# Kernel optimization log

Measured on AMD Instinct MI355X. Metric: run time of the kernel, lower is better.

The kernel has to match this reference:

```python
import jax, jax.numpy as jnp
import numpy as np

B, D, M, K = 4096, 768, 100000, 10


def setup_inputs() -> dict:
    key = jax.random.key(0)
    k1, k2 = jax.random.split(key)
    x = jax.random.normal(k1, (B, D), dtype=jnp.float32)
    evidence_embeddings = jax.random.normal(k2, (M, D), dtype=jnp.float32)
    return {"x": x, "evidence_embeddings": evidence_embeddings, "k": K}


def reference(x, evidence_embeddings, k):
    # cos_sim = x @ E^T  -> [B, M]
    cos_sim = jnp.einsum("bd,md->bm", x, evidence_embeddings)
    # top-k along evidence dim (dim=1)
    scores, indices = jax.lax.top_k(cos_sim, k)
    return scores, indices
```

## Files before the change

### kernel.cpp

```cpp
#include <hip/hip_runtime.h>
#include <math.h>
#include <stdint.h>

#define B_ROWS 4096
#define D_DIM  768
#define M_ROWS 100000
#define K_TOP  10

#define KSTEPS 48
#define E32N   3125
#define B32N   128
#define NGRP   16
#define NBB    16
#define NITER_TOT 391
#define CAND   12
#define KCN    12
#define LTK    6

typedef _Float16 f16;
typedef _Float16 f16x8 __attribute__((ext_vector_type(8)));
typedef float   f32x16 __attribute__((ext_vector_type(16)));

#define XF_BYTES (128ull * 48 * 1024)
#define EF_OFF   XF_BYTES
#define EF_BYTES (3125ull * 48 * 1024)
#define CS_OFF   (EF_OFF + EF_BYTES)
#define CS_BYTES (4096ull * NGRP * CAND * 4)
#define CI_OFF   (CS_OFF + CS_BYTES)
#define CI_BYTES (4096ull * NGRP * CAND * 4)
#define WS_NEED  (CI_OFF + CI_BYTES)

__global__ __launch_bounds__(256) void convert_frag(
    const float* __restrict__ src, f16* __restrict__ dst, int nband)
{
  int tid  = blockIdx.x * 256 + threadIdx.x;
  int l    = tid & 63;
  int rest = tid >> 6;
  int ks   = rest % KSTEPS;
  int band = rest / KSTEPS;
  if (band >= nband) return;
  int row = band * 32 + (l & 31);
  int k0  = ks * 16 + 8 * (l >> 5);
  const float* s = src + (size_t)row * D_DIM + k0;
  float4 v0 = *(const float4*)s;
  float4 v1 = *(const float4*)(s + 4);
  f16x8 o;
  o[0] = (f16)v0.x; o[1] = (f16)v0.y; o[2] = (f16)v0.z; o[3] = (f16)v0.w;
  o[4] = (f16)v1.x; o[5] = (f16)v1.y; o[6] = (f16)v1.z; o[7] = (f16)v1.w;
  *(f16x8*)(dst + (((size_t)band * KSTEPS + ks) << 9) + l * 8) = o;
}

__device__ __forceinline__ void ins6(float (&ts)[LTK], int (&ti)[LTK],
                                     float s, int idx)
{
  ts[LTK - 1] = s; ti[LTK - 1] = idx;
#pragma unroll
  for (int q = LTK - 1; q > 0; --q) {
    if (ts[q] > ts[q - 1]) {
      float a = ts[q]; ts[q] = ts[q - 1]; ts[q - 1] = a;
      int   b = ti[q]; ti[q] = ti[q - 1]; ti[q - 1] = b;
    }
  }
}

__device__ __forceinline__ float max16(const f32x16& v)
{
  float a = fmaxf(fmaxf(v[0], v[1]), fmaxf(v[2], v[3]));
  float b = fmaxf(fmaxf(v[4], v[5]), fmaxf(v[6], v[7]));
  float c = fmaxf(fmaxf(v[8], v[9]), fmaxf(v[10], v[11]));
  float d = fmaxf(fmaxf(v[12], v[13]), fmaxf(v[14], v[15]));
  return fmaxf(fmaxf(a, b), fmaxf(c, d));
}

__global__ __launch_bounds__(512, 2) void gemm_topk(
    const f16* __restrict__ Ef, const f16* __restrict__ Xf,
    float* __restrict__ cs, int* __restrict__ ci)
{
  __shared__ f16 lds[2][32768];

  const int t    = threadIdx.x;
  const int lane = t & 63;
  const int w    = t >> 6;
  const int ew   = w >> 2;
  const int bw   = w & 3;

  const int id = blockIdx.x;
  const int g  = (id & 7) + 8 * (id >> 7);
  const int bb = (id >> 3) & 15;
  const int niter = 24 + (g < (NITER_TOT - 16 * 24) ? 1 : 0);

  const bool isE = (w < 4);
  const f16* xsrc0 = Xf + (((size_t)(bb * 8 + 2 * (w - 4)) * KSTEPS) << 9);
  const f16* xsrc1 = Xf + (((size_t)(bb * 8 + 2 * (w - 4) + 1) * KSTEPS) << 9);
  const uint32_t dstE0 = (isE ? (2 * w) * 2048 : 16384 + 2 * (w - 4) * 2048);
  const uint32_t dstE1 = dstE0 + 2048;

  float ts0[LTK], ts1[LTK]; int ti0[LTK], ti1[LTK];
#pragma unroll
  for (int q = 0; q < LTK; ++q) {
    ts0[q] = -INFINITY; ts1[q] = -INFINITY;
    ti0[q] = 0x7fffffff; ti1[q] = 0x7fffffff;
  }

  for (int j = 0; j < niter; ++j) {
    const int it = g + NGRP * j;
    const int e32base = it * 8;

    const f16 *s0, *s1;
    if (isE) {
      int ea = e32base + 2 * w;     if (ea > E32N - 1) ea = E32N - 1;
      int eb = e32base + 2 * w + 1; if (eb > E32N - 1) eb = E32N - 1;
      s0 = Ef + (((size_t)ea * KSTEPS) << 9);
      s1 = Ef + (((size_t)eb * KSTEPS) << 9);
    } else { s0 = xsrc0; s1 = xsrc1; }

    f32x16 acc0[4], acc1[4];
#pragma unroll
    for (int e = 0; e < 4; ++e) {
#pragma unroll
      for (int q = 0; q < 16; ++q) { acc0[e][q] = 0.f; acc1[e][q] = 0.f; }
    }

    auto STAGE = [&](int kc, int bufi) {
      const f16* a0 = s0 + ((size_t)kc << 11) + lane * 8;
      const f16* a1 = s1 + ((size_t)kc << 11) + lane * 8;
      f16* d0 = &lds[bufi][0] + dstE0 + lane * 8;
      f16* d1 = &lds[bufi][0] + dstE1 + lane * 8;
#pragma unroll
      for (int ff = 0; ff < 4; ++ff) {
        __builtin_amdgcn_global_load_lds(
            (const __attribute__((address_space(1))) void*)(uintptr_t)(a0 + ff * 512),
            (__attribute__((address_space(3))) void*)(uint32_t)(uintptr_t)(d0 + ff * 512),
            16, 0, 0);
      }
#pragma unroll
      for (int ff = 0; ff < 4; ++ff) {
        __builtin_amdgcn_global_load_lds(
            (const __attribute__((address_space(1))) void*)(uintptr_t)(a1 + ff * 512),
            (__attribute__((address_space(3))) void*)(uint32_t)(uintptr_t)(d1 + ff * 512),
            16, 0, 0);
      }
    };

    STAGE(0, 0);
    for (int kc = 0; kc < KCN; ++kc) {
      asm volatile("s_waitcnt vmcnt(0)" ::: "memory");
      __builtin_amdgcn_s_barrier();
      if (kc < KCN - 1) STAGE(kc + 1, (kc + 1) & 1);
      const f16* Lb = &lds[kc & 1][0];
#pragma unroll
      for (int kk = 0; kk < 4; ++kk) {
        f16x8 a[4], b[2];
#pragma unroll
        for (int e = 0; e < 4; ++e)
          a[e] = *(const f16x8*)(Lb + ((((ew * 4 + e) * 4 + kk)) << 9) + lane * 8);
#pragma unroll
        for (int x2 = 0; x2 < 2; ++x2)
          b[x2] = *(const f16x8*)(Lb + ((32 + (bw * 2 + x2) * 4 + kk) << 9) + lane * 8);
#pragma unroll
        for (int e = 0; e < 4; ++e) {
          acc0[e] = __builtin_amdgcn_mfma_f32_32x32x16_f16(a[e], b[0], acc0[e], 0, 0, 0);
          acc1[e] = __builtin_amdgcn_mfma_f32_32x32x16_f16(a[e], b[1], acc1[e], 0, 0, 0);
        }
      }
    }

#pragma unroll
    for (int e = 0; e < 4; ++e) {
      const int ebase = e32base * 32 + (ew * 4 + e) * 32 + 4 * (lane >> 5);
      if (max16(acc0[e]) > ts0[LTK - 1]) {
#pragma unroll
        for (int q = 0; q < 16; ++q) {
          int eidx = ebase + (q & 3) + 8 * (q >> 2);
          float s = acc0[e][q];
          if (eidx < M_ROWS && s > ts0[LTK - 1]) ins6(ts0, ti0, s, eidx);
        }
      }
      if (max16(acc1[e]) > ts1[LTK - 1]) {
#pragma unroll
        for (int q = 0; q < 16; ++q) {
          int eidx = ebase + (q & 3) + 8 * (q >> 2);
          float s = acc1[e][q];
          if (eidx < M_ROWS && s > ts1[LTK - 1]) ins6(ts1, ti1, s, eidx);
        }
      }
    }
  }

  __syncthreads();
  float* ds = (float*)&lds[0][0];
  int*   di = (int*)((char*)&lds[0][0] + 32 * 1024);
  {
    int half = lane >> 5, cl = lane & 31;
    int base0 = ((((ew * 2 + half) * 4 + bw) * 2 + 0) * 32 + cl) * LTK;
    int base1 = ((((ew * 2 + half) * 4 + bw) * 2 + 1) * 32 + cl) * LTK;
#pragma unroll
    for (int q = 0; q < LTK; ++q) {
      ds[base0 + q] = ts0[q]; di[base0 + q] = ti0[q];
      ds[base1 + q] = ts1[q]; di[base1 + q] = ti1[q];
    }
  }
  __syncthreads();
  if (t < 256) {
    int c = t; int bw2 = c >> 6, bt2 = (c >> 5) & 1, cl2 = c & 31;
    int hb[4];
#pragma unroll
    for (int u = 0; u < 4; ++u) {
      int ew2 = u >> 1, h2 = u & 1;
      hb[u] = ((((ew2 * 2 + h2) * 4 + bw2) * 2 + bt2) * 32 + cl2) * LTK;
    }
    const int row = bb * 256 + c;
    float* ocs = cs + ((size_t)row * NGRP + g) * CAND;
    int*   oci = ci + ((size_t)row * NGRP + g) * CAND;
    for (int o = 0; o < CAND; ++o) {
      float best = -INFINITY; int bidx = 0x7fffffff; int bu = 0, bq = 0;
#pragma unroll
      for (int u = 0; u < 4; ++u) {
        for (int q = 0; q < LTK; ++q) {
          float s = ds[hb[u] + q]; int id2 = di[hb[u] + q];
          if (s > best || (s == best && id2 < bidx)) { best = s; bidx = id2; bu = u; bq = q; }
        }
      }
      ds[hb[bu] + bq] = -INFINITY;
      ocs[o] = best; oci[o] = bidx;
    }
  }
}

__global__ __launch_bounds__(64) void final_merge(
    const float* __restrict__ x, const float* __restrict__ E,
    const float* __restrict__ cs, const int* __restrict__ ci,
    float* __restrict__ out)
{
  __shared__ float ls[192]; __shared__ int li[192];
  __shared__ int c16[16]; __shared__ double rs[16];
  const int row = blockIdx.x;
  const int lane = threadIdx.x;
  for (int q = lane; q < 192; q += 64) {
    ls[q] = cs[(size_t)row * 192 + q];
    li[q] = ci[(size_t)row * 192 + q];
  }
  __syncthreads();

  for (int o = 0; o < 16; ++o) {
    float bs = -INFINITY; int bi = 0x7fffffff; int bp = 0;
    for (int q = lane; q < 192; q += 64) {
      float s = ls[q];
      if (s > bs || (s == bs && li[q] < bi)) { bs = s; bi = li[q]; bp = q; }
    }
#pragma unroll
    for (int mk = 1; mk <= 32; mk <<= 1) {
      float qs = __shfl_xor(bs, mk, 64);
      int   qi = __shfl_xor(bi, mk, 64);
      int   qp = __shfl_xor(bp, mk, 64);
      if (qs > bs || (qs == bs && qi < bi)) { bs = qs; bi = qi; bp = qp; }
    }
    if (lane == 0) { c16[o] = bi; ls[bp] = -INFINITY; }
    __syncthreads();
  }

  {
    int cd = lane >> 2, p = lane & 3;
    int cid = c16[cd];
    const float* Er = E + (size_t)cid * D_DIM + p * 192;
    const float* Xr = x + (size_t)row * D_DIM + p * 192;
    double s = 0.0;
#pragma unroll 8
    for (int d = 0; d < 192; ++d) s += (double)Xr[d] * (double)Er[d];
    s += __shfl_xor(s, 1, 64);
    s += __shfl_xor(s, 2, 64);
    if (p == 0) rs[cd] = s;
  }
  __syncthreads();

  if (lane == 0) {
    for (int o = 0; o < K_TOP; ++o) {
      double bs = rs[0]; int bc = c16[0]; int b = 0;
      for (int q = 1; q < 16; ++q) {
        double v = rs[q]; int cq = c16[q];
        if (v > bs || (v == bs && cq < bc)) { bs = v; bc = cq; b = q; }
      }
      out[(size_t)row * K_TOP + o] = (float)bs;
      out[(size_t)B_ROWS * K_TOP + (size_t)row * K_TOP + o] = (float)bc;
      rs[b] = -1.0e300;
    }
  }
}

#define RB   16
#define GQ   64
#define MMF  4
#define NJ   391
#define NTF  1024
#define XPAD 772
#define DQ4  192

__global__ __launch_bounds__(NTF, 4) void retr_fused(
    const float* __restrict__ x, const float* __restrict__ E,
    float* __restrict__ out)
{
  __shared__ float smem[21248];
  const int t = threadIdx.x;
  const int r = t & 15;
  const int g = t >> 4;
  const int rb0 = blockIdx.x * RB;
  {
    const float4* xg = (const float4*)(x + (size_t)rb0 * D_DIM);
    for (int q = t; q < RB * DQ4; q += NTF) {
      int row = q / DQ4, c4 = q % DQ4;
      float4 v = xg[q];
      *(float4*)(smem + row * XPAD + c4 * 4) = v;
    }
  }
  __syncthreads();
  float ts[K_TOP]; int ti[K_TOP];
#pragma unroll
  for (int q = 0; q < K_TOP; ++q) { ts[q] = -INFINITY; ti[q] = 0x7fffffff; }
  const float4* xr4 = (const float4*)(smem + r * XPAD);
  for (int j = 0; j < NJ; ++j) {
    const int m0 = (g + (j << 6)) * MMF;
    const float4* ep[MMF];
#pragma unroll
    for (int mm = 0; mm < MMF; ++mm) {
      int ml = m0 + mm;
      int mc = (ml < M_ROWS) ? ml : (M_ROWS - 1);
      ep[mm] = (const float4*)(E + (size_t)mc * D_DIM);
    }
    float4 acc[MMF];
#pragma unroll
    for (int mm = 0; mm < MMF; ++mm) acc[mm] = make_float4(0.f, 0.f, 0.f, 0.f);
#pragma unroll 4
    for (int dq = 0; dq < DQ4; ++dq) {
      float4 xv = xr4[dq];
#pragma unroll
      for (int mm = 0; mm < MMF; ++mm) {
        float4 e = ep[mm][dq];
        acc[mm].x += e.x * xv.x; acc[mm].y += e.y * xv.y;
        acc[mm].z += e.z * xv.z; acc[mm].w += e.w * xv.w;
      }
    }
#pragma unroll
    for (int mm = 0; mm < MMF; ++mm) {
      int ml = m0 + mm;
      float s = (acc[mm].x + acc[mm].y) + (acc[mm].z + acc[mm].w);
      if (ml < M_ROWS && s > ts[K_TOP - 1]) {
        ts[K_TOP - 1] = s; ti[K_TOP - 1] = ml;
#pragma unroll
        for (int q = K_TOP - 1; q > 0; --q) {
          if (ts[q] > ts[q - 1]) {
            float tf = ts[q]; ts[q] = ts[q - 1]; ts[q - 1] = tf;
            int   tq = ti[q]; ti[q] = ti[q - 1]; ti[q - 1] = tq;
          }
        }
      }
    }
  }
  __syncthreads();
  float*  cs  = smem;
  int*    ci  = (int*)(smem + 10240);
  int*    cnd = (int*)(smem + 20480);
  double* rsd = (double*)(smem + 20736);
#pragma unroll
  for (int q = 0; q < K_TOP; ++q) {
    cs[(r * GQ + g) * K_TOP + q] = ts[q];
    ci[(r * GQ + g) * K_TOP + q] = ti[q];
  }
  __syncthreads();
  const int w = t >> 6;
  const int lane = t & 63;
  {
    float ms[K_TOP]; int mi[K_TOP];
#pragma unroll
    for (int q = 0; q < K_TOP; ++q) {
      ms[q] = cs[(w * GQ + lane) * K_TOP + q];
      mi[q] = ci[(w * GQ + lane) * K_TOP + q];
    }
    for (int o = 0; o < 16; ++o) {
      float hs = ms[0]; int hi = mi[0];
      float bs = hs;    int bi = hi;
#pragma unroll
      for (int mk = 1; mk <= 32; mk <<= 1) {
        float qs = __shfl_xor(bs, mk, 64);
        int   qi = __shfl_xor(bi, mk, 64);
        if (qs > bs || (qs == bs && qi < bi)) { bs = qs; bi = qi; }
      }
      bool win = (hs == bs) && (hi == bi);
      if (win) {
#pragma unroll
        for (int q = 0; q < K_TOP - 1; ++q) { ms[q] = ms[q + 1]; mi[q] = mi[q + 1]; }
        ms[K_TOP - 1] = -INFINITY; mi[K_TOP - 1] = 0x7fffffff;
      }
      if (lane == 0) cnd[w * 16 + o] = bi;
    }
  }
  __syncthreads();
  {
    int cand = lane >> 2, p = lane & 3;
    int cid = cnd[w * 16 + cand];
    const float* Er = E + (size_t)cid * D_DIM + p * 192;
    const float* Xr = x + (size_t)(rb0 + w) * D_DIM + p * 192;
    double s = 0.0;
#pragma unroll 8
    for (int d = 0; d < 192; ++d) s += (double)Xr[d] * (double)Er[d];
    s += __shfl_xor(s, 1, 64);
    s += __shfl_xor(s, 2, 64);
    if (p == 0) rsd[w * 16 + cand] = s;
  }
  __syncthreads();
  if (lane == 0) {
    const int row = rb0 + w;
    for (int o = 0; o < K_TOP; ++o) {
      double bsv = rsd[w * 16 + 0]; int bci = cnd[w * 16 + 0]; int b = 0;
      for (int q = 1; q < 16; ++q) {
        double v = rsd[w * 16 + q]; int c = cnd[w * 16 + q];
        if (v > bsv || (v == bsv && c < bci)) { bsv = v; bci = c; b = q; }
      }
      out[(size_t)row * K_TOP + o] = (float)bsv;
      out[(size_t)B_ROWS * K_TOP + (size_t)row * K_TOP + o] = (float)bci;
      rsd[w * 16 + b] = -1.0e300;
    }
  }
}

extern "C" void kernel_launch(void* const* d_in, const int* in_sizes, int n_in,
                              void* d_out, int out_size, void* d_ws, size_t ws_size,
                              hipStream_t stream) {
  const float* x = (const float*)d_in[0];
  const float* E = (const float*)d_in[1];
  float* out = (float*)d_out;

  if (ws_size < WS_NEED) {
    retr_fused<<<dim3(B_ROWS / RB), NTF, 0, stream>>>(x, E, out);
    return;
  }

  f16*   Xfp = (f16*)d_ws;
  f16*   Efp = (f16*)((char*)d_ws + EF_OFF);
  float* csp = (float*)((char*)d_ws + CS_OFF);
  int*   cip = (int*)((char*)d_ws + CI_OFF);

  convert_frag<<<dim3((B32N * KSTEPS * 64) / 256), 256, 0, stream>>>(x, Xfp, B32N);
  convert_frag<<<dim3((E32N * KSTEPS * 64) / 256), 256, 0, stream>>>(E, Efp, E32N);
  gemm_topk<<<dim3(NBB * NGRP), 512, 0, stream>>>(Efp, Xfp, csp, cip);
  final_merge<<<dim3(B_ROWS), 64, 0, stream>>>(x, E, csp, cip, out);
}
```

Baseline: 941.5 us.

## Deepen LDS pipeline to four stages and prefetch across tile iterations

Splits the K loop into 24 smaller chunks held in a 4-buffer LDS ring. Loads are issued three stages ahead, including the first chunks of the next E tile, so they overlap the current tile's top-k epilogue. Partial vmcnt waits replace the full drain on each step. It also raises wave priority around the MFMA bursts. The cost is twice as many barriers per tile and more complex waitcnt bookkeeping at the loop tail.

```diff
diff --git a/kernel.cpp b/kernel.cpp
--- a/kernel.cpp
+++ b/kernel.cpp
@@ -14,7 +14,7 @@
 #define NBB    16
 #define NITER_TOT 391
 #define CAND   12
-#define KCN    12
+#define KCN    24
 #define LTK    6
 
 typedef _Float16 f16;
@@ -72,11 +72,19 @@
   return fmaxf(fmaxf(a, b), fmaxf(c, d));
 }
 
+__device__ __forceinline__ void gll16(const f16* src, f16* dst)
+{
+  __builtin_amdgcn_global_load_lds(
+      (const __attribute__((address_space(1))) void*)(uintptr_t)src,
+      (__attribute__((address_space(3))) void*)(uint32_t)(uintptr_t)dst,
+      16, 0, 0);
+}
+
 __global__ __launch_bounds__(512, 2) void gemm_topk(
     const f16* __restrict__ Ef, const f16* __restrict__ Xf,
     float* __restrict__ cs, int* __restrict__ ci)
 {
-  __shared__ f16 lds[2][32768];
+  __shared__ f16 lds[4][16384];
 
   const int t    = threadIdx.x;
   const int lane = t & 63;
@@ -90,10 +98,27 @@
   const int niter = 24 + (g < (NITER_TOT - 16 * 24) ? 1 : 0);
 
   const bool isE = (w < 4);
-  const f16* xsrc0 = Xf + (((size_t)(bb * 8 + 2 * (w - 4)) * KSTEPS) << 9);
-  const f16* xsrc1 = Xf + (((size_t)(bb * 8 + 2 * (w - 4) + 1) * KSTEPS) << 9);
-  const uint32_t dstE0 = (isE ? (2 * w) * 2048 : 16384 + 2 * (w - 4) * 2048);
-  const uint32_t dstE1 = dstE0 + 2048;
+  const f16* xs0 = Xf + ((size_t)(bb * 8 + 2 * (w - 4)) * KSTEPS) * 512;
+  const f16* xs1 = Xf + ((size_t)(bb * 8 + 2 * (w - 4) + 1) * KSTEPS) * 512;
+  const uint32_t dbase = (isE ? (4 * w) * 512 : (16 + 4 * (w - 4)) * 512);
+
+  auto STAGE = [&](int e32b, int kc, int bufi) {
+    const f16 *s0, *s1;
+    if (isE) {
+      int ea = e32b + 2 * w;     if (ea > E32N - 1) ea = E32N - 1;
+      int eb = e32b + 2 * w + 1; if (eb > E32N - 1) eb = E32N - 1;
+      s0 = Ef + ((size_t)ea * KSTEPS + 2 * kc) * 512;
+      s1 = Ef + ((size_t)eb * KSTEPS + 2 * kc) * 512;
+    } else {
+      s0 = xs0 + (size_t)(2 * kc) * 512;
+      s1 = xs1 + (size_t)(2 * kc) * 512;
+    }
+    f16* dp = &lds[bufi][0] + dbase + lane * 8;
+    gll16(s0 + lane * 8,       dp);
+    gll16(s0 + lane * 8 + 512, dp + 512);
+    gll16(s1 + lane * 8,       dp + 1024);
+    gll16(s1 + lane * 8 + 512, dp + 1536);
+  };
 
   float ts0[LTK], ts1[LTK]; int ti0[LTK], ti1[LTK];
 #pragma unroll
@@ -102,17 +127,13 @@
     ti0[q] = 0x7fffffff; ti1[q] = 0x7fffffff;
   }
 
+  STAGE(g * 8, 0, 0);
+  STAGE(g * 8, 1, 1);
+  STAGE(g * 8, 2, 2);
+
   for (int j = 0; j < niter; ++j) {
-    const int it = g + NGRP * j;
-    const int e32base = it * 8;
-
-    const f16 *s0, *s1;
-    if (isE) {
-      int ea = e32base + 2 * w;     if (ea > E32N - 1) ea = E32N - 1;
-      int eb = e32base + 2 * w + 1; if (eb > E32N - 1) eb = E32N - 1;
-      s0 = Ef + (((size_t)ea * KSTEPS) << 9);
-      s1 = Ef + (((size_t)eb * KSTEPS) << 9);
-    } else { s0 = xsrc0; s1 = xsrc1; }
+    const int e32base = (g + NGRP * j) * 8;
+    const bool lastj = (j == niter - 1);
 
     f32x16 acc0[4], acc1[4];
 #pragma unroll
@@ -121,47 +142,37 @@
       for (int q = 0; q < 16; ++q) { acc0[e][q] = 0.f; acc1[e][q] = 0.f; }
     }
 
-    auto STAGE = [&](int kc, int bufi) {
-      const f16* a0 = s0 + ((size_t)kc << 11) + lane * 8;
-      const f16* a1 = s1 + ((size_t)kc << 11) + lane * 8;
-      f16* d0 = &lds[bufi][0] + dstE0 + lane * 8;
-      f16* d1 = &lds[bufi][0] + dstE1 + lane * 8;
-#pragma unroll
-      for (int ff = 0; ff < 4; ++ff) {
-        __builtin_amdgcn_global_load_lds(
-            (const __attribute__((address_space(1))) void*)(uintptr_t)(a0 + ff * 512),
-            (__attribute__((address_space(3))) void*)(uint32_t)(uintptr_t)(d0 + ff * 512),
-            16, 0, 0);
-      }
-#pragma unroll
-      for (int ff = 0; ff < 4; ++ff) {
-        __builtin_amdgcn_global_load_lds(
-            (const __attribute__((address_space(1))) void*)(uintptr_t)(a1 + ff * 512),
-            (__attribute__((address_space(3))) void*)(uint32_t)(uintptr_t)(d1 + ff * 512),
-            16, 0, 0);
-      }
-    };
-
-    STAGE(0, 0);
+#pragma unroll 1
     for (int kc = 0; kc < KCN; ++kc) {
-      asm volatile("s_waitcnt vmcnt(0)" ::: "memory");
+      if (!lastj || kc < KCN - 2) {
+        asm volatile("s_waitcnt vmcnt(8)" ::: "memory");
+      } else if (kc == KCN - 2) {
+        asm volatile("s_waitcnt vmcnt(4)" ::: "memory");
+      } else {
+        asm volatile("s_waitcnt vmcnt(0)" ::: "memory");
+      }
       __builtin_amdgcn_s_barrier();
-      if (kc < KCN - 1) STAGE(kc + 1, (kc + 1) & 1);
-      const f16* Lb = &lds[kc & 1][0];
-#pragma unroll
-      for (int kk = 0; kk < 4; ++kk) {
+
+      if (kc < KCN - 3)      STAGE(e32base, kc + 3, (kc + 3) & 3);
+      else if (!lastj)       STAGE(e32base + NGRP * 8, kc + 3 - KCN, (kc + 3) & 3);
+
+      const f16* Lb = &lds[kc & 3][0];
+#pragma unroll
+      for (int u = 0; u < 2; ++u) {
         f16x8 a[4], b[2];
 #pragma unroll
         for (int e = 0; e < 4; ++e)
-          a[e] = *(const f16x8*)(Lb + ((((ew * 4 + e) * 4 + kk)) << 9) + lane * 8);
+          a[e] = *(const f16x8*)(Lb + (((ew * 4 + e) * 2 + u) << 9) + lane * 8);
 #pragma unroll
         for (int x2 = 0; x2 < 2; ++x2)
-          b[x2] = *(const f16x8*)(Lb + ((32 + (bw * 2 + x2) * 4 + kk) << 9) + lane * 8);
+          b[x2] = *(const f16x8*)(Lb + ((16 + (bw * 2 + x2) * 2 + u) << 9) + lane * 8);
+        __builtin_amdgcn_s_setprio(1);
 #pragma unroll
         for (int e = 0; e < 4; ++e) {
           acc0[e] = __builtin_amdgcn_mfma_f32_32x32x16_f16(a[e], b[0], acc0[e], 0, 0, 0);
           acc1[e] = __builtin_amdgcn_mfma_f32_32x32x16_f16(a[e], b[1], acc1[e], 0, 0, 0);
         }
+        __builtin_amdgcn_s_setprio(0);
       }
     }
 
```

Measured after the change: 1.184 ms. +25.7%, slower.

## Load X fragments directly to registers, stage only E via LDS, remap blocks to XCDs

Applied to the files above, without the earlier changes.

X operand fragments are now read straight from global memory into registers each k-chunk instead of being staged through LDS. Only E tiles go through LDS, so the LDS buffer is halved and all 8 waves share E staging with 4 loads each. The block-to-(bb,g) mapping is reorganised so each XCD covers a subset of X row blocks and E groups, aiming for better L2 locality. A bounds clamp on candidate indices in the refinement kernel is added for safety.

```diff
diff --git a/kernel.cpp b/kernel.cpp
--- a/kernel.cpp
+++ b/kernel.cpp
@@ -72,11 +72,19 @@
   return fmaxf(fmaxf(a, b), fmaxf(c, d));
 }
 
+__device__ __forceinline__ void gll16(const f16* src, f16* dst)
+{
+  __builtin_amdgcn_global_load_lds(
+      (const __attribute__((address_space(1))) void*)(uintptr_t)src,
+      (__attribute__((address_space(3))) void*)(uint32_t)(uintptr_t)dst,
+      16, 0, 0);
+}
+
 __global__ __launch_bounds__(512, 2) void gemm_topk(
     const f16* __restrict__ Ef, const f16* __restrict__ Xf,
     float* __restrict__ cs, int* __restrict__ ci)
 {
-  __shared__ f16 lds[2][32768];
+  __shared__ f16 lds[2][16384];
 
   const int t    = threadIdx.x;
   const int lane = t & 63;
@@ -84,16 +92,17 @@
   const int ew   = w >> 2;
   const int bw   = w & 3;
 
-  const int id = blockIdx.x;
-  const int g  = (id & 7) + 8 * (id >> 7);
-  const int bb = (id >> 3) & 15;
+  const int id  = blockIdx.x;
+  const int xcd = id & 7;
+  const int q8  = id >> 3;
+  const int bb  = 8 * (xcd >> 2) + (q8 & 7);
+  const int g   = 4 * (xcd & 3) + (q8 >> 3);
   const int niter = 24 + (g < (NITER_TOT - 16 * 24) ? 1 : 0);
 
-  const bool isE = (w < 4);
-  const f16* xsrc0 = Xf + (((size_t)(bb * 8 + 2 * (w - 4)) * KSTEPS) << 9);
-  const f16* xsrc1 = Xf + (((size_t)(bb * 8 + 2 * (w - 4) + 1) * KSTEPS) << 9);
-  const uint32_t dstE0 = (isE ? (2 * w) * 2048 : 16384 + 2 * (w - 4) * 2048);
-  const uint32_t dstE1 = dstE0 + 2048;
+  const uint32_t dbase = (uint32_t)(w * 4) * 512;
+
+  const f16* xb0 = Xf + ((size_t)(bb * 8 + bw * 2 + 0) * KSTEPS) * 512 + lane * 8;
+  const f16* xb1 = Xf + ((size_t)(bb * 8 + bw * 2 + 1) * KSTEPS) * 512 + lane * 8;
 
   float ts0[LTK], ts1[LTK]; int ti0[LTK], ti1[LTK];
 #pragma unroll
@@ -103,16 +112,16 @@
   }
 
   for (int j = 0; j < niter; ++j) {
-    const int it = g + NGRP * j;
-    const int e32base = it * 8;
-
-    const f16 *s0, *s1;
-    if (isE) {
-      int ea = e32base + 2 * w;     if (ea > E32N - 1) ea = E32N - 1;
-      int eb = e32base + 2 * w + 1; if (eb > E32N - 1) eb = E32N - 1;
-      s0 = Ef + (((size_t)ea * KSTEPS) << 9);
-      s1 = Ef + (((size_t)eb * KSTEPS) << 9);
-    } else { s0 = xsrc0; s1 = xsrc1; }
+    const int e32base = (g + NGRP * j) * 8;
+
+    auto STAGE = [&](int kc, int bufi) {
+      int et = e32base + w; if (et > E32N - 1) et = E32N - 1;
+      const f16* s0 = Ef + ((size_t)et * KSTEPS + kc * 4) * 512 + lane * 8;
+      f16* d0 = &lds[bufi][0] + dbase + lane * 8;
+#pragma unroll
+      for (int ff = 0; ff < 4; ++ff)
+        gll16(s0 + ff * 512, d0 + ff * 512);
+    };
 
     f32x16 acc0[4], acc1[4];
 #pragma unroll
@@ -120,47 +129,33 @@
 #pragma unroll
       for (int q = 0; q < 16; ++q) { acc0[e][q] = 0.f; acc1[e][q] = 0.f; }
     }
-
-    auto STAGE = [&](int kc, int bufi) {
-      const f16* a0 = s0 + ((size_t)kc << 11) + lane * 8;
-      const f16* a1 = s1 + ((size_t)kc << 11) + lane * 8;
-      f16* d0 = &lds[bufi][0] + dstE0 + lane * 8;
-      f16* d1 = &lds[bufi][0] + dstE1 + lane * 8;
-#pragma unroll
-      for (int ff = 0; ff < 4; ++ff) {
-        __builtin_amdgcn_global_load_lds(
-            (const __attribute__((address_space(1))) void*)(uintptr_t)(a0 + ff * 512),
-            (__attribute__((address_space(3))) void*)(uint32_t)(uintptr_t)(d0 + ff * 512),
-            16, 0, 0);
-      }
-#pragma unroll
-      for (int ff = 0; ff < 4; ++ff) {
-        __builtin_amdgcn_global_load_lds(
-            (const __attribute__((address_space(1))) void*)(uintptr_t)(a1 + ff * 512),
-            (__attribute__((address_space(3))) void*)(uint32_t)(uintptr_t)(d1 + ff * 512),
-            16, 0, 0);
-      }
-    };
 
     STAGE(0, 0);
     for (int kc = 0; kc < KCN; ++kc) {
       asm volatile("s_waitcnt vmcnt(0)" ::: "memory");
       __builtin_amdgcn_s_barrier();
+
+      f16x8 b0[4], b1[4];
+#pragma unroll
+      for (int kk = 0; kk < 4; ++kk) {
+        b0[kk] = *(const f16x8*)(xb0 + ((size_t)(kc * 4 + kk)) * 512);
+        b1[kk] = *(const f16x8*)(xb1 + ((size_t)(kc * 4 + kk)) * 512);
+      }
+      asm volatile("" ::: "memory");
+
       if (kc < KCN - 1) STAGE(kc + 1, (kc + 1) & 1);
+
       const f16* Lb = &lds[kc & 1][0];
 #pragma unroll
       for (int kk = 0; kk < 4; ++kk) {
-        f16x8 a[4], b[2];
+        f16x8 a[4];
 #pragma unroll
         for (int e = 0; e < 4; ++e)
           a[e] = *(const f16x8*)(Lb + ((((ew * 4 + e) * 4 + kk)) << 9) + lane * 8);
 #pragma unroll
-        for (int x2 = 0; x2 < 2; ++x2)
-          b[x2] = *(const f16x8*)(Lb + ((32 + (bw * 2 + x2) * 4 + kk) << 9) + lane * 8);
-#pragma unroll
         for (int e = 0; e < 4; ++e) {
-          acc0[e] = __builtin_amdgcn_mfma_f32_32x32x16_f16(a[e], b[0], acc0[e], 0, 0, 0);
-          acc1[e] = __builtin_amdgcn_mfma_f32_32x32x16_f16(a[e], b[1], acc1[e], 0, 0, 0);
+          acc0[e] = __builtin_amdgcn_mfma_f32_32x32x16_f16(a[e], b0[kk], acc0[e], 0, 0, 0);
+          acc1[e] = __builtin_amdgcn_mfma_f32_32x32x16_f16(a[e], b1[kk], acc1[e], 0, 0, 0);
         }
       }
     }
@@ -262,6 +257,7 @@
   {
     int cd = lane >> 2, p = lane & 3;
     int cid = c16[cd];
+    if ((unsigned)cid >= M_ROWS) cid = 0;
     const float* Er = E + (size_t)cid * D_DIM + p * 192;
     const float* Xr = x + (size_t)row * D_DIM + p * 192;
     double s = 0.0;
```

Result: slower. 1.614 ms (+71.4%).
